# Kernel tuning notes

Hardware: AMD Instinct MI355X
Metric: run time of the kernel (lower is better)

## Reference

```python
import jax, jax.numpy as jnp
import numpy as np

NUM_HEADS = 8

def _ln(x, w, b, eps=1e-5):
    m = x.mean(-1, keepdims=True)
    v = ((x - m) ** 2).mean(-1, keepdims=True)
    return (x - m) / jnp.sqrt(v + eps) * w + b

def _l2n(x, axis=-1, eps=1e-12):
    n = jnp.linalg.norm(x, axis=axis, keepdims=True)
    return x / jnp.maximum(n, eps)

def setup_inputs() -> dict:
    key = jax.random.key(0)
    ks = jax.random.split(key, 30)
    B, N, C, nc, t = 2, 4096, 256, 150, 3
    Hh = Ww = 64
    hid = 4 * C
    s = 0.02
    inp = {}
    inp['x'] = jax.random.normal(ks[0], (B, N, C), jnp.float32)
    inp['z'] = jax.random.normal(ks[1], (B, nc, (t + 1) * N), jnp.float32)
    inp['mem'] = jax.random.normal(ks[2], (B * t, N, C), jnp.float32)
    inp['clustering_w'] = s * jax.random.normal(ks[3], (nc, C), jnp.float32)
    inp['prompt1'] = jax.random.normal(ks[4], (nc,), jnp.float32)
    inp['tdt1'] = jnp.eye(nc, dtype=jnp.float32) + s * jax.random.normal(ks[5], (nc, nc), jnp.float32)
    inp['prompt2'] = jax.random.normal(ks[6], (nc,), jnp.float32)
    inp['tdt2'] = jnp.eye(nc, dtype=jnp.float32) + s * jax.random.normal(ks[7], (nc, nc), jnp.float32)
    inp['sim_alpha'] = jnp.ones((1,), jnp.float32)
    inp['sim_beta'] = jnp.zeros((1,), jnp.float32)
    inp['q_w'] = s * jax.random.normal(ks[8], (C, C), jnp.float32)
    inp['q_b'] = s * jax.random.normal(ks[9], (C,), jnp.float32)
    inp['k_w'] = s * jax.random.normal(ks[10], (C, C), jnp.float32)
    inp['k_b'] = s * jax.random.normal(ks[11], (C,), jnp.float32)
    inp['v_w'] = s * jax.random.normal(ks[12], (C, C), jnp.float32)
    inp['v_b'] = s * jax.random.normal(ks[13], (C,), jnp.float32)
    inp['proj_w'] = s * jax.random.normal(ks[14], (C, C), jnp.float32)
    inp['proj_b'] = s * jax.random.normal(ks[15], (C,), jnp.float32)
    inp['norm_w'] = jnp.ones((C,), jnp.float32)
    inp['norm_b'] = jnp.zeros((C,), jnp.float32)
    inp['fc1_w'] = s * jax.random.normal(ks[16], (hid, C), jnp.float32)
    inp['fc1_b'] = s * jax.random.normal(ks[17], (hid,), jnp.float32)
    inp['dw_w'] = s * jax.random.normal(ks[18], (hid, 1, 3, 3), jnp.float32)
    inp['dw_b'] = s * jax.random.normal(ks[19], (hid,), jnp.float32)
    inp['fc2_w'] = s * jax.random.normal(ks[20], (C, hid), jnp.float32)
    inp['fc2_b'] = s * jax.random.normal(ks[21], (C,), jnp.float32)
    inp['H'] = Hh
    inp['W'] = Ww
    inp['t'] = t
    return inp

def _forward(x, z, mem, clustering_w, prompt1, tdt1, prompt2, tdt2, sim_alpha, sim_beta,
             q_w, q_b, k_w, k_b, v_w, v_b, proj_w, proj_b, norm_w, norm_b,
             fc1_w, fc1_b, dw_w, dw_b, fc2_w, fc2_b, H, W, t):
    B, N, C = x.shape
    nc = clustering_w.shape[0]
    res = x
    T = t + 1
    # cat memory frames with current frame: [(B*T), N, C]
    xf = jnp.concatenate([mem.reshape(B, t, N, C), x[:, None]], axis=1).reshape(B * T, N, C)
    # clustering head: (SRPS approximated as identity) 1x1 conv dim->num_clusters
    cl = jnp.einsum('bnc,kc->bkn', xf, clustering_w)            # [(B*T), nc, N]
    cl = cl.reshape(B, T, nc, N).transpose(0, 2, 1, 3).reshape(B, nc, T * N)
    # top-down prompt modulation of z and cluster logits
    zc = z.transpose(0, 2, 1)                                   # [B, T*N, nc]
    cos = _l2n(zc, -1) @ _l2n(prompt1[None, :, None], axis=1)   # [B, T*N, 1]
    zc = (zc * jnp.clip(cos, 0.0, 1.0)) @ tdt1
    clc = cl.transpose(0, 2, 1)
    cos = _l2n(clc, -1) @ _l2n(prompt2[None, :, None], axis=1)
    clc = (clc * jnp.clip(cos, 0.0, 1.0)) @ tdt2
    cluster_x_z = ((clc + zc) * 0.5).transpose(0, 2, 1)          # [B, nc, T*N]
    # inner_center: per-frame soft assignment -> cluster centers
    center = cluster_x_z.reshape(B, nc, T, N).transpose(0, 2, 1, 3)  # [B, T, nc, N]
    assigned_results = center
    soft = jax.nn.softmax(center, axis=-1)
    cx = xf.reshape(B, T, N, C)
    cen = jnp.einsum('btkn,btnc->btkc', soft, cx)               # [B, T, nc, C]
    last, prev = cen[:, -1], cen[:, :-1]                        # [B,nc,C], [B,t,nc,C]
    dot = jnp.einsum('bkc,btkc->btk', last, prev)
    denom = jnp.maximum(jnp.linalg.norm(last, axis=-1)[:, None] * jnp.linalg.norm(prev, axis=-1), 1e-8)
    gate = jax.nn.sigmoid(sim_beta + sim_alpha * (dot / denom))  # [B, t, nc]
    C_in = last + (gate[..., None] * prev).sum(axis=1)          # [B, nc, C]
    C_in = _ln(C_in, norm_w, norm_b)
    # cross attention: tokens query cluster centers
    hd = C // NUM_HEADS
    q = (res @ q_w.T + q_b) * (1.0 / np.sqrt(hd))
    k = C_in @ k_w.T + k_b
    v = C_in @ v_w.T + v_b
    q = q.reshape(B, N, NUM_HEADS, hd).transpose(0, 2, 1, 3)
    k = k.reshape(B, nc, NUM_HEADS, hd).transpose(0, 2, 1, 3)
    v = v.reshape(B, nc, NUM_HEADS, hd).transpose(0, 2, 1, 3)
    attn = jax.nn.softmax(jnp.einsum('bhnd,bhkd->bhnk', q, k), axis=-1)
    o = jnp.einsum('bhnk,bhkd->bhnd', attn, v).transpose(0, 2, 1, 3).reshape(B, N, C)
    o = o @ proj_w.T + proj_b
    out = res + _ln(o, norm_w, norm_b)
    # MLP with depthwise conv
    h = out @ fc1_w.T + fc1_b                                   # [B, N, 4C]
    hid = h.shape[-1]
    h_img = h.transpose(0, 2, 1).reshape(B, hid, H, W)
    h_img = jax.lax.conv_general_dilated(h_img, dw_w, (1, 1), 'SAME',
                                         feature_group_count=hid,
                                         dimension_numbers=('NCHW', 'OIHW', 'NCHW'))
    h_img = h_img + dw_b[None, :, None, None]
    h = h_img.reshape(B, hid, N).transpose(0, 2, 1)
    h = jax.nn.gelu(h, approximate=False) @ fc2_w.T + fc2_b
    out = out + _ln(h, norm_w, norm_b)
    return out, cluster_x_z, assigned_results

def reference(x, z, mem, clustering_w, prompt1, tdt1, prompt2, tdt2, sim_alpha, sim_beta,
              q_w, q_b, k_w, k_b, v_w, v_b, proj_w, proj_b, norm_w, norm_b,
              fc1_w, fc1_b, dw_w, dw_b, fc2_w, fc2_b, H, W, t):
    return _forward(x, z, mem, clustering_w, prompt1, tdt1, prompt2, tdt2, sim_alpha, sim_beta,
                    q_w, q_b, k_w, k_b, v_w, v_b, proj_w, proj_b, norm_w, norm_b,
                    fc1_w, fc1_b, dw_w, dw_b, fc2_w, fc2_b, H, W, t)
```

## Files before the change

kernel.cpp:

```cpp
#include <hip/hip_runtime.h>
#include <math.h>


typedef __attribute__((ext_vector_type(8))) short bf16x8;
typedef __attribute__((ext_vector_type(4))) short bf16x4;
typedef __attribute__((ext_vector_type(4))) float f32x4;

__device__ __forceinline__ short f2b(float f) {
  union { float f; unsigned int u; } c; c.f = f;
  unsigned int r = (c.u + 0x7fffu + ((c.u >> 16) & 1u)) >> 16;
  return (short)r;
}

__device__ __forceinline__ float bred_sum(float v, float* red) {
  int tid = threadIdx.x;
  red[tid] = v; __syncthreads();
  #pragma unroll
  for (int s = 128; s > 0; s >>= 1) {
    if (tid < s) red[tid] += red[tid + s];
    __syncthreads();
  }
  float r = red[0]; __syncthreads();
  return r;
}

__global__ __launch_bounds__(256) void gemm_mfma(
    const float* __restrict__ A, const float* __restrict__ W,
    const float* __restrict__ bias, float* __restrict__ out,
    int M, int N, int K, float alpha)
{
  __shared__ __align__(16) short As[64 * 72];
  __shared__ __align__(16) short Bs[64 * 72];
  const int tid = threadIdx.x;
  const int m0 = blockIdx.x * 64;
  const int n0 = blockIdx.y * 64;
  const int wave = tid >> 6;
  const int lane = tid & 63;
  const int wm = wave & 1, wn = wave >> 1;
  const int t16 = lane & 15;
  const int k8 = (lane >> 4) * 8;

  f32x4 acc[2][2];
  #pragma unroll
  for (int i = 0; i < 2; ++i)
    #pragma unroll
    for (int j = 0; j < 2; ++j)
      acc[i][j] = (f32x4){0.f, 0.f, 0.f, 0.f};

  const int sr = tid >> 2;
  const int sk = (tid & 3) * 16;

  for (int k0 = 0; k0 < K; k0 += 64) {
    {
      const float* ap = &A[(size_t)(m0 + sr) * K + k0 + sk];
      float4 v0 = *(const float4*)&ap[0];
      float4 v1 = *(const float4*)&ap[4];
      float4 v2 = *(const float4*)&ap[8];
      float4 v3 = *(const float4*)&ap[12];
      bf16x8 w0, w1;
      w0[0] = f2b(v0.x); w0[1] = f2b(v0.y); w0[2] = f2b(v0.z); w0[3] = f2b(v0.w);
      w0[4] = f2b(v1.x); w0[5] = f2b(v1.y); w0[6] = f2b(v1.z); w0[7] = f2b(v1.w);
      w1[0] = f2b(v2.x); w1[1] = f2b(v2.y); w1[2] = f2b(v2.z); w1[3] = f2b(v2.w);
      w1[4] = f2b(v3.x); w1[5] = f2b(v3.y); w1[6] = f2b(v3.z); w1[7] = f2b(v3.w);
      *(bf16x8*)&As[sr * 72 + sk] = w0;
      *(bf16x8*)&As[sr * 72 + sk + 8] = w1;
    }
    {
      const float* wp = &W[(size_t)(n0 + sr) * K + k0 + sk];
      float4 v0 = *(const float4*)&wp[0];
      float4 v1 = *(const float4*)&wp[4];
      float4 v2 = *(const float4*)&wp[8];
      float4 v3 = *(const float4*)&wp[12];
      bf16x8 w0, w1;
      w0[0] = f2b(v0.x); w0[1] = f2b(v0.y); w0[2] = f2b(v0.z); w0[3] = f2b(v0.w);
      w0[4] = f2b(v1.x); w0[5] = f2b(v1.y); w0[6] = f2b(v1.z); w0[7] = f2b(v1.w);
      w1[0] = f2b(v2.x); w1[1] = f2b(v2.y); w1[2] = f2b(v2.z); w1[3] = f2b(v2.w);
      w1[4] = f2b(v3.x); w1[5] = f2b(v3.y); w1[6] = f2b(v3.z); w1[7] = f2b(v3.w);
      *(bf16x8*)&Bs[sr * 72 + sk] = w0;
      *(bf16x8*)&Bs[sr * 72 + sk + 8] = w1;
    }
    __syncthreads();
    #pragma unroll
    for (int ks = 0; ks < 2; ++ks) {
      const int kofs = ks * 32 + k8;
      bf16x8 af0 = *(const bf16x8*)&As[(wm * 32 +  0 + t16) * 72 + kofs];
      bf16x8 af1 = *(const bf16x8*)&As[(wm * 32 + 16 + t16) * 72 + kofs];
      bf16x8 bf0 = *(const bf16x8*)&Bs[(wn * 32 +  0 + t16) * 72 + kofs];
      bf16x8 bf1 = *(const bf16x8*)&Bs[(wn * 32 + 16 + t16) * 72 + kofs];
      acc[0][0] = __builtin_amdgcn_mfma_f32_16x16x32_bf16(af0, bf0, acc[0][0], 0, 0, 0);
      acc[1][0] = __builtin_amdgcn_mfma_f32_16x16x32_bf16(af1, bf0, acc[1][0], 0, 0, 0);
      acc[0][1] = __builtin_amdgcn_mfma_f32_16x16x32_bf16(af0, bf1, acc[0][1], 0, 0, 0);
      acc[1][1] = __builtin_amdgcn_mfma_f32_16x16x32_bf16(af1, bf1, acc[1][1], 0, 0, 0);
    }
    __syncthreads();
  }
  const int r4 = (lane >> 4) * 4;
  #pragma unroll
  for (int ni = 0; ni < 2; ++ni) {
    const int gcol = n0 + wn * 32 + ni * 16 + t16;
    const float bb = bias[gcol];
    #pragma unroll
    for (int mi = 0; mi < 2; ++mi) {
      #pragma unroll
      for (int r = 0; r < 4; ++r) {
        const int gm = m0 + wm * 32 + mi * 16 + r4 + r;
        out[(size_t)gm * N + gcol] = alpha * (acc[mi][ni][r] + bb);
      }
    }
  }
}

__global__ __launch_bounds__(256) void gemm_ln_res(
    const float* __restrict__ A, const float* __restrict__ W,
    const float* __restrict__ bias, const float* __restrict__ res,
    const float* __restrict__ nw, const float* __restrict__ nb,
    float* __restrict__ dst, int K)
{
  __shared__ __align__(16) short As[16 * 72];
  __shared__ __align__(16) short Bs[256 * 72];
  __shared__ float red[16][4][2];
  const int tid = threadIdx.x;
  const int m0 = blockIdx.x * 16;
  const int wave = tid >> 6, lane = tid & 63;
  const int t16 = lane & 15, quad = lane >> 4, k8 = quad * 8;

  f32x4 acc[4];
  #pragma unroll
  for (int i = 0; i < 4; ++i) acc[i] = (f32x4){0.f, 0.f, 0.f, 0.f};

  const int sr = tid >> 2;
  const int sk = (tid & 3) * 16;
  const int arow = tid >> 4, akc = (tid & 15) * 4;

  for (int k0 = 0; k0 < K; k0 += 64) {
    {
      float4 v = *(const float4*)&A[(size_t)(m0 + arow) * K + k0 + akc];
      bf16x4 w;
      w[0] = f2b(v.x); w[1] = f2b(v.y); w[2] = f2b(v.z); w[3] = f2b(v.w);
      *(bf16x4*)&As[arow * 72 + akc] = w;
    }
    #pragma unroll
    for (int p = 0; p < 4; ++p) {
      const float* wp = &W[(size_t)(p * 64 + sr) * K + k0 + sk];
      float4 v0 = *(const float4*)&wp[0];
      float4 v1 = *(const float4*)&wp[4];
      float4 v2 = *(const float4*)&wp[8];
      float4 v3 = *(const float4*)&wp[12];
      bf16x8 w0, w1;
      w0[0] = f2b(v0.x); w0[1] = f2b(v0.y); w0[2] = f2b(v0.z); w0[3] = f2b(v0.w);
      w0[4] = f2b(v1.x); w0[5] = f2b(v1.y); w0[6] = f2b(v1.z); w0[7] = f2b(v1.w);
      w1[0] = f2b(v2.x); w1[1] = f2b(v2.y); w1[2] = f2b(v2.z); w1[3] = f2b(v2.w);
      w1[4] = f2b(v3.x); w1[5] = f2b(v3.y); w1[6] = f2b(v3.z); w1[7] = f2b(v3.w);
      *(bf16x8*)&Bs[(p * 64 + sr) * 72 + sk] = w0;
      *(bf16x8*)&Bs[(p * 64 + sr) * 72 + sk + 8] = w1;
    }
    __syncthreads();
    #pragma unroll
    for (int ks = 0; ks < 2; ++ks) {
      const int kofs = ks * 32 + k8;
      bf16x8 af = *(const bf16x8*)&As[t16 * 72 + kofs];
      #pragma unroll
      for (int ni = 0; ni < 4; ++ni) {
        bf16x8 bf = *(const bf16x8*)&Bs[(wave * 64 + ni * 16 + t16) * 72 + kofs];
        acc[ni] = __builtin_amdgcn_mfma_f32_16x16x32_bf16(af, bf, acc[ni], 0, 0, 0);
      }
    }
    __syncthreads();
  }

  const int gcolb = wave * 64;
  float val[4][4];
  float s[4] = {0.f, 0.f, 0.f, 0.f}, s2[4] = {0.f, 0.f, 0.f, 0.f};
  #pragma unroll
  for (int ni = 0; ni < 4; ++ni) {
    const float bb = bias[gcolb + ni * 16 + t16];
    #pragma unroll
    for (int r = 0; r < 4; ++r) {
      float v = acc[ni][r] + bb;
      val[ni][r] = v;
      s[r] += v;
      s2[r] = fmaf(v, v, s2[r]);
    }
  }
  #pragma unroll
  for (int off = 1; off < 16; off <<= 1) {
    #pragma unroll
    for (int r = 0; r < 4; ++r) {
      s[r] += __shfl_xor(s[r], off);
      s2[r] += __shfl_xor(s2[r], off);
    }
  }
  if (t16 == 0) {
    #pragma unroll
    for (int r = 0; r < 4; ++r) {
      red[quad * 4 + r][wave][0] = s[r];
      red[quad * 4 + r][wave][1] = s2[r];
    }
  }
  __syncthreads();
  float mu[4], inv[4];
  #pragma unroll
  for (int r = 0; r < 4; ++r) {
    const int row = quad * 4 + r;
    float st  = red[row][0][0] + red[row][1][0] + red[row][2][0] + red[row][3][0];
    float st2 = red[row][0][1] + red[row][1][1] + red[row][2][1] + red[row][3][1];
    float m = st * (1.f / 256.f);
    mu[r] = m;
    inv[r] = rsqrtf(st2 * (1.f / 256.f) - m * m + 1e-5f);
  }
  #pragma unroll
  for (int ni = 0; ni < 4; ++ni) {
    const int gcol = gcolb + ni * 16 + t16;
    const float wc = nw[gcol], bc = nb[gcol];
    #pragma unroll
    for (int r = 0; r < 4; ++r) {
      const int gm = m0 + quad * 4 + r;
      dst[(size_t)gm * 256 + gcol] =
          res[(size_t)gm * 256 + gcol] + (val[ni][r] - mu[r]) * inv[r] * wc + bc;
    }
  }
}

__global__ __launch_bounds__(256) void prep_bt(
    const float* __restrict__ cw, const float* __restrict__ tdt2, const float* __restrict__ tdt1,
    short* __restrict__ cwb, short* __restrict__ TT)
{
  int idx = blockIdx.x * 256 + threadIdx.x;
  if (idx < 160 * 256) {
    int kc = idx >> 8, k = idx & 255;
    float v = (kc < 150) ? cw[kc * 256 + k] : 0.f;
    cwb[idx] = f2b(v);
  }
  if (idx < 160 * 320) {
    int kc = idx / 320, kk = idx - kc * 320;
    float t = 0.f;
    if (kc < 150) {
      if (kk < 150) t = tdt2[kk * 150 + kc];
      else if (kk >= 160 && kk < 310) t = tdt1[(kk - 160) * 150 + kc];
    }
    TT[idx] = f2b(t);
  }
}

__global__ __launch_bounds__(256) void xf_t(
    const float* __restrict__ x, const float* __restrict__ mem, short* __restrict__ xfT)
{
  __shared__ float tile[64][257];
  const int bt = blockIdx.y;
  const int n0 = blockIdx.x * 64;
  const int b = bt >> 2, ti = bt & 3;
  const float* xf = (ti < 3) ? (mem + (size_t)(b * 3 + ti) * 4096 * 256)
                             : (x + (size_t)b * 4096 * 256);
  const int tid = threadIdx.x;
  const int r = tid >> 2, cofs = (tid & 3) * 64;
  const float* src = xf + (size_t)(n0 + r) * 256 + cofs;
  #pragma unroll
  for (int i = 0; i < 16; ++i) {
    float4 v = *(const float4*)&src[i * 4];
    tile[r][cofs + i * 4 + 0] = v.x;
    tile[r][cofs + i * 4 + 1] = v.y;
    tile[r][cofs + i * 4 + 2] = v.z;
    tile[r][cofs + i * 4 + 3] = v.w;
  }
  __syncthreads();
  short* dst = xfT + ((size_t)bt * 256 + tid) * 4096 + n0;
  #pragma unroll
  for (int seg = 0; seg < 8; ++seg) {
    bf16x8 w;
    #pragma unroll
    for (int j = 0; j < 8; ++j) w[j] = f2b(tile[seg * 8 + j][tid]);
    *(bf16x8*)&dst[seg * 8] = w;
  }
}

__global__ __launch_bounds__(256) void fused_csz(
    const float* __restrict__ x, const float* __restrict__ mem, const float* __restrict__ z,
    const short* __restrict__ cwb, const short* __restrict__ TT,
    const float* __restrict__ p1, const float* __restrict__ p2,
    float* __restrict__ csz, float* __restrict__ asg)
{
  __shared__ __align__(16) short Acatile[64 * 328];
  __shared__ float p1s[160], p2s[160];
  __shared__ float sred[4][16][9];
  __shared__ float czs[64];
  const int tid = threadIdx.x;
  const int r0 = blockIdx.x * 64;
  const int b = r0 >> 14;
  const int mmg = r0 & 16383;
  const int ti = mmg >> 12, nn = mmg & 4095;
  const float* Ab = ((ti < 3) ? (mem + (size_t)(b * 3 + ti) * 4096 * 256)
                              : (x + (size_t)b * 4096 * 256)) + (size_t)nn * 256;
  const int wave = tid >> 6, lane = tid & 63;
  const int t16 = lane & 15, quad = lane >> 4, k8 = quad * 8;

  const int kr = tid >> 4, c4 = (tid & 15) * 4;
  float4 zv[10];
  #pragma unroll
  for (int it = 0; it < 10; ++it) {
    const int k = it * 16 + kr;
    zv[it] = make_float4(0.f, 0.f, 0.f, 0.f);
    if (k < 150) zv[it] = *(const float4*)&z[((size_t)b * 150 + k) * 16384 + mmg + c4];
  }
  if (tid < 160) {
    p2s[tid] = (tid < 150) ? p2[tid] : 0.f;
    p1s[tid] = (tid < 150) ? p1[tid] : 0.f;
  }

  f32x4 acc[10];
  #pragma unroll
  for (int i = 0; i < 10; ++i) acc[i] = (f32x4){0.f, 0.f, 0.f, 0.f};
  {
    const float* ap = Ab + (size_t)(wave * 16 + t16) * 256 + k8;
    const short* bp = cwb + t16 * 256 + k8;
    #pragma unroll 2
    for (int ks = 0; ks < 8; ++ks) {
      float4 v0 = *(const float4*)&ap[ks * 32];
      float4 v1 = *(const float4*)&ap[ks * 32 + 4];
      bf16x8 a;
      a[0] = f2b(v0.x); a[1] = f2b(v0.y); a[2] = f2b(v0.z); a[3] = f2b(v0.w);
      a[4] = f2b(v1.x); a[5] = f2b(v1.y); a[6] = f2b(v1.z); a[7] = f2b(v1.w);
      #pragma unroll
      for (int nf = 0; nf < 10; ++nf) {
        bf16x8 bv = *(const bf16x8*)&bp[nf * 4096 + ks * 32];
        acc[nf] = __builtin_amdgcn_mfma_f32_16x16x32_bf16(a, bv, acc[nf], 0, 0, 0);
      }
    }
  }
  __syncthreads();

  {
    float d[4] = {0.f, 0.f, 0.f, 0.f}, s[4] = {0.f, 0.f, 0.f, 0.f};
    float pn = 0.f;
    #pragma unroll
    for (int nf = 0; nf < 10; ++nf) {
      float a2 = p2s[nf * 16 + t16];
      pn += a2 * a2;
      #pragma unroll
      for (int r = 0; r < 4; ++r) {
        float v = acc[nf][r];
        d[r] = fmaf(v, a2, d[r]);
        s[r] = fmaf(v, v, s[r]);
      }
    }
    #pragma unroll
    for (int off = 1; off < 16; off <<= 1) {
      pn += __shfl_xor(pn, off);
      #pragma unroll
      for (int r = 0; r < 4; ++r) {
        d[r] += __shfl_xor(d[r], off);
        s[r] += __shfl_xor(s[r], off);
      }
    }
    const float spn = fmaxf(sqrtf(pn), 1e-12f);
    float cs[4];
    #pragma unroll
    for (int r = 0; r < 4; ++r) {
      float c = d[r] / (fmaxf(sqrtf(s[r]), 1e-12f) * spn);
      cs[r] = fminf(fmaxf(c, 0.f), 1.f);
    }
    #pragma unroll
    for (int nf = 0; nf < 10; ++nf)
      #pragma unroll
      for (int r = 0; r < 4; ++r)
        Acatile[(wave * 16 + quad * 4 + r) * 328 + nf * 16 + t16] = f2b(acc[nf][r] * cs[r]);
  }

  {
    float d[4] = {0.f, 0.f, 0.f, 0.f}, sv[4] = {0.f, 0.f, 0.f, 0.f};
    float pn = 0.f;
    #pragma unroll
    for (int it = 0; it < 10; ++it) {
      const int k = it * 16 + kr;
      const float a = p1s[k];
      d[0] = fmaf(zv[it].x, a, d[0]); d[1] = fmaf(zv[it].y, a, d[1]);
      d[2] = fmaf(zv[it].z, a, d[2]); d[3] = fmaf(zv[it].w, a, d[3]);
      sv[0] = fmaf(zv[it].x, zv[it].x, sv[0]); sv[1] = fmaf(zv[it].y, zv[it].y, sv[1]);
      sv[2] = fmaf(zv[it].z, zv[it].z, sv[2]); sv[3] = fmaf(zv[it].w, zv[it].w, sv[3]);
      pn = fmaf(a, a, pn);
    }
    #pragma unroll
    for (int off = 16; off < 64; off <<= 1) {
      pn += __shfl_xor(pn, off);
      #pragma unroll
      for (int r = 0; r < 4; ++r) {
        d[r] += __shfl_xor(d[r], off);
        sv[r] += __shfl_xor(sv[r], off);
      }
    }
    if ((lane >> 4) == 0) {
      #pragma unroll
      for (int r = 0; r < 4; ++r) {
        sred[wave][lane][r] = d[r];
        sred[wave][lane][4 + r] = sv[r];
      }
      sred[wave][lane][8] = pn;
    }
  }
  __syncthreads();
  if (tid < 64) {
    const int cg = tid >> 2, r = tid & 3;
    float dd = 0.f, ss = 0.f, pp = 0.f;
    #pragma unroll
    for (int w = 0; w < 4; ++w) {
      dd += sred[w][cg][r];
      ss += sred[w][cg][4 + r];
      pp += sred[w][cg][8];
    }
    float c = dd / (fmaxf(sqrtf(ss), 1e-12f) * fmaxf(sqrtf(pp), 1e-12f));
    czs[tid] = fminf(fmaxf(c, 0.f), 1.f);
  }
  __syncthreads();
  {
    const float cz0 = czs[c4 + 0], cz1 = czs[c4 + 1], cz2 = czs[c4 + 2], cz3 = czs[c4 + 3];
    #pragma unroll
    for (int it = 0; it < 10; ++it) {
      const int k = it * 16 + kr;
      Acatile[(c4 + 0) * 328 + 160 + k] = f2b(zv[it].x * cz0);
      Acatile[(c4 + 1) * 328 + 160 + k] = f2b(zv[it].y * cz1);
      Acatile[(c4 + 2) * 328 + 160 + k] = f2b(zv[it].z * cz2);
      Acatile[(c4 + 3) * 328 + 160 + k] = f2b(zv[it].w * cz3);
    }
  }
  __syncthreads();

  {
    const int wm = wave & 1, wn = wave >> 1;
    f32x4 c2[2][5];
    #pragma unroll
    for (int i = 0; i < 2; ++i)
      #pragma unroll
      for (int j = 0; j < 5; ++j)
        c2[i][j] = (f32x4){0.f, 0.f, 0.f, 0.f};
    const short* bp = TT + (size_t)(wn * 80 + t16) * 320 + k8;
    #pragma unroll 2
    for (int ks = 0; ks < 10; ++ks) {
      bf16x8 a0 = *(const bf16x8*)&Acatile[(wm * 32 + t16) * 328 + ks * 32 + k8];
      bf16x8 a1 = *(const bf16x8*)&Acatile[(wm * 32 + 16 + t16) * 328 + ks * 32 + k8];
      #pragma unroll
      for (int nf = 0; nf < 5; ++nf) {
        bf16x8 bv = *(const bf16x8*)&bp[nf * 5120 + ks * 32];
        c2[0][nf] = __builtin_amdgcn_mfma_f32_16x16x32_bf16(a0, bv, c2[0][nf], 0, 0, 0);
        c2[1][nf] = __builtin_amdgcn_mfma_f32_16x16x32_bf16(a1, bv, c2[1][nf], 0, 0, 0);
      }
    }
    #pragma unroll
    for (int nf = 0; nf < 5; ++nf) {
      const int kc = wn * 80 + nf * 16 + t16;
      if (kc < 150) {
        #pragma unroll
        for (int mf = 0; mf < 2; ++mf) {
          const int moff = wm * 32 + mf * 16 + quad * 4;
          float4 r4;
          r4.x = 0.5f * c2[mf][nf][0];
          r4.y = 0.5f * c2[mf][nf][1];
          r4.z = 0.5f * c2[mf][nf][2];
          r4.w = 0.5f * c2[mf][nf][3];
          *(float4*)&csz[((size_t)b * 150 + kc) * 16384 + mmg + moff] = r4;
          *(float4*)&asg[(((size_t)b * 4 + ti) * 150 + kc) * 4096 + nn + moff] = r4;
        }
      }
    }
  }
}

__global__ __launch_bounds__(256) void softmax_stats_e(
    const float* __restrict__ csz, float* __restrict__ lr_, short* __restrict__ ecsz)
{
  __shared__ float wred[8];
  const int row = blockIdx.x;
  const int bt = row / 150, k = row - bt * 150;
  const int b = bt >> 2, ti = bt & 3;
  const float* p = csz + ((size_t)b * 150 + k) * 16384 + ti * 4096;
  const int base = threadIdx.x * 16;
  float4 v[4];
  #pragma unroll
  for (int i = 0; i < 4; ++i) v[i] = *(const float4*)&p[base + i * 4];
  float mx = -1e30f;
  #pragma unroll
  for (int i = 0; i < 4; ++i)
    mx = fmaxf(mx, fmaxf(fmaxf(v[i].x, v[i].y), fmaxf(v[i].z, v[i].w)));
  #pragma unroll
  for (int off = 1; off < 64; off <<= 1) mx = fmaxf(mx, __shfl_xor(mx, off));
  const int wave = threadIdx.x >> 6, lane = threadIdx.x & 63;
  if (lane == 0) wred[wave] = mx;
  __syncthreads();
  mx = fmaxf(fmaxf(wred[0], wred[1]), fmaxf(wred[2], wred[3]));
  const float L = 1.4426950408889634f;
  float s = 0.f;
  bf16x8 e0, e1;
  #pragma unroll
  for (int i = 0; i < 2; ++i) {
    float a = exp2f((v[i].x - mx) * L);
    float bq = exp2f((v[i].y - mx) * L);
    float cq = exp2f((v[i].z - mx) * L);
    float dq = exp2f((v[i].w - mx) * L);
    s += a + bq + cq + dq;
    e0[i * 4 + 0] = f2b(a); e0[i * 4 + 1] = f2b(bq); e0[i * 4 + 2] = f2b(cq); e0[i * 4 + 3] = f2b(dq);
  }
  #pragma unroll
  for (int i = 2; i < 4; ++i) {
    float a = exp2f((v[i].x - mx) * L);
    float bq = exp2f((v[i].y - mx) * L);
    float cq = exp2f((v[i].z - mx) * L);
    float dq = exp2f((v[i].w - mx) * L);
    s += a + bq + cq + dq;
    e1[(i - 2) * 4 + 0] = f2b(a); e1[(i - 2) * 4 + 1] = f2b(bq);
    e1[(i - 2) * 4 + 2] = f2b(cq); e1[(i - 2) * 4 + 3] = f2b(dq);
  }
  #pragma unroll
  for (int off = 1; off < 64; off <<= 1) s += __shfl_xor(s, off);
  if (lane == 0) wred[4 + wave] = s;
  __syncthreads();
  short* er = ecsz + ((size_t)bt * 160 + k) * 4096 + base;
  *(bf16x8*)&er[0] = e0;
  *(bf16x8*)&er[8] = e1;
  if (threadIdx.x == 0) lr_[row] = wred[4] + wred[5] + wred[6] + wred[7];
}

__global__ __launch_bounds__(256) void gemm_cen_at(
    const short* __restrict__ ecsz, const short* __restrict__ xfT,
    float* __restrict__ cen)
{
  __shared__ __align__(16) short As[160 * 136];
  const int tid = threadIdx.x;
  const int chalf = blockIdx.x;
  const int bt = blockIdx.y;
  const int sp = blockIdx.z;
  const int n0 = sp * 128;
  const int wave = tid >> 6, lane = tid & 63;
  const int t16 = lane & 15, quad = lane >> 4, k8 = quad * 8;
  const int cbase = chalf * 128 + wave * 32;

  f32x4 acc[10][2];
  #pragma unroll
  for (int i = 0; i < 10; ++i) {
    acc[i][0] = (f32x4){0.f, 0.f, 0.f, 0.f};
    acc[i][1] = (f32x4){0.f, 0.f, 0.f, 0.f};
  }

  const short* erow = ecsz + (size_t)bt * 160 * 4096 + n0;
  #pragma unroll
  for (int p = 0; p < 10; ++p) {
    const int g = p * 256 + tid;
    const int row = g >> 4;
    const int col8 = (g & 15) * 8;
    *(bf16x8*)&As[row * 136 + col8] = *(const bf16x8*)&erow[(size_t)row * 4096 + col8];
  }
  __syncthreads();
  const short* xrow = xfT + (size_t)bt * 256 * 4096 + n0;
  #pragma unroll
  for (int kc = 0; kc < 4; ++kc) {
    bf16x8 b0 = *(const bf16x8*)&xrow[(size_t)(cbase + t16) * 4096 + kc * 32 + k8];
    bf16x8 b1 = *(const bf16x8*)&xrow[(size_t)(cbase + 16 + t16) * 4096 + kc * 32 + k8];
    #pragma unroll
    for (int mt = 0; mt < 10; ++mt) {
      bf16x8 aA = *(const bf16x8*)&As[(mt * 16 + t16) * 136 + kc * 32 + k8];
      acc[mt][0] = __builtin_amdgcn_mfma_f32_16x16x32_bf16(aA, b0, acc[mt][0], 0, 0, 0);
      acc[mt][1] = __builtin_amdgcn_mfma_f32_16x16x32_bf16(aA, b1, acc[mt][1], 0, 0, 0);
    }
  }
  #pragma unroll
  for (int mt = 0; mt < 10; ++mt) {
    #pragma unroll
    for (int r = 0; r < 4; ++r) {
      const int grow = mt * 16 + quad * 4 + r;
      if (grow < 150) {
        atomicAdd(&cen[((size_t)bt * 150 + grow) * 256 + cbase + t16], acc[mt][0][r]);
        atomicAdd(&cen[((size_t)bt * 150 + grow) * 256 + cbase + 16 + t16], acc[mt][1][r]);
      }
    }
  }
}

__global__ __launch_bounds__(256) void gate_ln(
    const float* __restrict__ cen, const float* __restrict__ lr_,
    const float* __restrict__ alpha_, const float* __restrict__ beta_,
    const float* __restrict__ nw, const float* __restrict__ nb, float* __restrict__ cin)
{
  __shared__ float red[256];
  int bk = blockIdx.x;
  int b = bk / 150, k = bk % 150;
  int c = threadIdx.x;
  const float* base = cen + ((size_t)b * 4 * 150) * 256;
  const float* lrb = lr_ + (size_t)b * 4 * 150;
  float lc  = base[((size_t)3 * 150 + k) * 256 + c] / lrb[3 * 150 + k];
  float p0  = base[((size_t)0 * 150 + k) * 256 + c] / lrb[0 * 150 + k];
  float p1v = base[((size_t)1 * 150 + k) * 256 + c] / lrb[1 * 150 + k];
  float p2v = base[((size_t)2 * 150 + k) * 256 + c] / lrb[2 * 150 + k];
  float nl = bred_sum(lc * lc, red);
  float q0 = bred_sum(p0 * p0, red);
  float q1 = bred_sum(p1v * p1v, red);
  float q2 = bred_sum(p2v * p2v, red);
  float d0 = bred_sum(lc * p0, red);
  float d1 = bred_sum(lc * p1v, red);
  float d2 = bred_sum(lc * p2v, red);
  float al = alpha_[0], be = beta_[0];
  float snl = sqrtf(nl);
  float g0 = 1.f / (1.f + expf(-(be + al * (d0 / fmaxf(snl * sqrtf(q0), 1e-8f)))));
  float g1 = 1.f / (1.f + expf(-(be + al * (d1 / fmaxf(snl * sqrtf(q1), 1e-8f)))));
  float g2 = 1.f / (1.f + expf(-(be + al * (d2 / fmaxf(snl * sqrtf(q2), 1e-8f)))));
  float ci = lc + g0 * p0 + g1 * p1v + g2 * p2v;
  float mu = bred_sum(ci, red) * (1.f / 256.f);
  float df = ci - mu;
  float var = bred_sum(df * df, red) * (1.f / 256.f);
  cin[(size_t)bk * 256 + c] = df * rsqrtf(var + 1e-5f) * nw[c] + nb[c];
}

__global__ __launch_bounds__(256) void gemm_nt(
    const float* __restrict__ A, const float* __restrict__ W,
    const float* __restrict__ bias, float* __restrict__ out,
    int M, int N, int K, float alpha)
{
  __shared__ __align__(16) float As[16][132];
  __shared__ __align__(16) float Ws[16][68];
  const int tid = threadIdx.x;
  const int m0 = blockIdx.x * 128;
  const int n0 = blockIdx.y * 64;
  const int tm = tid & 15;
  const int tn = tid >> 4;
  float acc[8][4];
  #pragma unroll
  for (int i = 0; i < 8; ++i)
    #pragma unroll
    for (int j = 0; j < 4; ++j) acc[i][j] = 0.f;

  const int lr = tid >> 2;
  const int lk = (tid & 3) * 4;

  for (int k0 = 0; k0 < K; k0 += 16) {
    #pragma unroll
    for (int p = 0; p < 2; ++p) {
      int r = lr + p * 64;
      int gm = m0 + r;
      float4 v = make_float4(0.f, 0.f, 0.f, 0.f);
      if (gm < M) v = *(const float4*)&A[(size_t)gm * K + k0 + lk];
      As[lk + 0][r] = v.x; As[lk + 1][r] = v.y; As[lk + 2][r] = v.z; As[lk + 3][r] = v.w;
    }
    {
      float4 v = *(const float4*)&W[(size_t)(n0 + lr) * K + k0 + lk];
      Ws[lk + 0][lr] = v.x; Ws[lk + 1][lr] = v.y; Ws[lk + 2][lr] = v.z; Ws[lk + 3][lr] = v.w;
    }
    __syncthreads();
    #pragma unroll
    for (int kk = 0; kk < 16; ++kk) {
      float4 a0 = *(const float4*)&As[kk][tm * 8];
      float4 a1 = *(const float4*)&As[kk][tm * 8 + 4];
      float4 w0 = *(const float4*)&Ws[kk][tn * 4];
      float av[8] = {a0.x, a0.y, a0.z, a0.w, a1.x, a1.y, a1.z, a1.w};
      float wv[4] = {w0.x, w0.y, w0.z, w0.w};
      #pragma unroll
      for (int i = 0; i < 8; ++i)
        #pragma unroll
        for (int j = 0; j < 4; ++j)
          acc[i][j] = fmaf(av[i], wv[j], acc[i][j]);
    }
    __syncthreads();
  }
  float4 bv = *(const float4*)&bias[n0 + tn * 4];
  float bb[4] = {bv.x, bv.y, bv.z, bv.w};
  #pragma unroll
  for (int i = 0; i < 8; ++i) {
    int gm = m0 + tm * 8 + i;
    if (gm >= M) continue;
    float4 r;
    r.x = alpha * (acc[i][0] + bb[0]);
    r.y = alpha * (acc[i][1] + bb[1]);
    r.z = alpha * (acc[i][2] + bb[2]);
    r.w = alpha * (acc[i][3] + bb[3]);
    *(float4*)&out[(size_t)gm * N + n0 + tn * 4] = r;
  }
}

__global__ __launch_bounds__(256) void attn_mfma(
    const float* __restrict__ q, const float* __restrict__ ks, const float* __restrict__ vs,
    float* __restrict__ o)
{
  __shared__ __align__(16) short Ps[128 * 168];
  __shared__ __align__(16) short VT[32 * 168];
  __shared__ float lrow[128];
  const int tid = threadIdx.x;
  const int bid = blockIdx.x;
  const int ntile = bid & 31;
  const int bh = bid >> 5;
  const int b = bh >> 3, h = bh & 7;
  const int n0 = ntile * 128;
  const int wave = tid >> 6, lane = tid & 63;
  const int t16 = lane & 15, quad = lane >> 4;
  const int k8 = quad * 8;
  const int wr = wave * 32;

  for (int i = tid; i < 5120; i += 256) {
    int d = i / 160, kc = i - d * 160;
    VT[d * 168 + kc] = (kc < 150) ? f2b(vs[((size_t)b * 150 + kc) * 256 + h * 32 + d]) : (short)0;
  }

  bf16x8 aQ[2];
  #pragma unroll
  for (int mt = 0; mt < 2; ++mt) {
    const float* qp = &q[((size_t)b * 4096 + n0 + wr + mt * 16 + t16) * 256 + h * 32 + k8];
    float4 v0 = *(const float4*)&qp[0];
    float4 v1 = *(const float4*)&qp[4];
    bf16x8 w;
    w[0] = f2b(v0.x); w[1] = f2b(v0.y); w[2] = f2b(v0.z); w[3] = f2b(v0.w);
    w[4] = f2b(v1.x); w[5] = f2b(v1.y); w[6] = f2b(v1.z); w[7] = f2b(v1.w);
    aQ[mt] = w;
  }

  f32x4 s[2][10];
  #pragma unroll
  for (int ct = 0; ct < 10; ++ct) {
    const int c = ct * 16 + t16;
    bf16x8 bK = {0, 0, 0, 0, 0, 0, 0, 0};
    if (c < 150) {
      const float* kp = &ks[((size_t)b * 150 + c) * 256 + h * 32 + k8];
      float4 v0 = *(const float4*)&kp[0];
      float4 v1 = *(const float4*)&kp[4];
      bK[0] = f2b(v0.x); bK[1] = f2b(v0.y); bK[2] = f2b(v0.z); bK[3] = f2b(v0.w);
      bK[4] = f2b(v1.x); bK[5] = f2b(v1.y); bK[6] = f2b(v1.z); bK[7] = f2b(v1.w);
    }
    f32x4 zero = (f32x4){0.f, 0.f, 0.f, 0.f};
    s[0][ct] = __builtin_amdgcn_mfma_f32_16x16x32_bf16(aQ[0], bK, zero, 0, 0, 0);
    s[1][ct] = __builtin_amdgcn_mfma_f32_16x16x32_bf16(aQ[1], bK, zero, 0, 0, 0);
  }

  #pragma unroll
  for (int mt = 0; mt < 2; ++mt) {
    #pragma unroll
    for (int r = 0; r < 4; ++r) {
      float mx = -1e30f;
      #pragma unroll
      for (int ct = 0; ct < 10; ++ct) {
        float v = s[mt][ct][r];
        if (ct == 9 && t16 >= 6) { v = -1e30f; s[mt][ct][r] = v; }
        mx = fmaxf(mx, v);
      }
      mx = fmaxf(mx, __shfl_xor(mx, 1));
      mx = fmaxf(mx, __shfl_xor(mx, 2));
      mx = fmaxf(mx, __shfl_xor(mx, 4));
      mx = fmaxf(mx, __shfl_xor(mx, 8));
      float ls = 0.f;
      #pragma unroll
      for (int ct = 0; ct < 10; ++ct) {
        float e = expf(s[mt][ct][r] - mx);
        s[mt][ct][r] = e;
        ls += e;
      }
      ls += __shfl_xor(ls, 1);
      ls += __shfl_xor(ls, 2);
      ls += __shfl_xor(ls, 4);
      ls += __shfl_xor(ls, 8);
      if (t16 == 0) lrow[wr + mt * 16 + quad * 4 + r] = 1.f / ls;
      #pragma unroll
      for (int ct = 0; ct < 10; ++ct)
        Ps[(wr + mt * 16 + quad * 4 + r) * 168 + ct * 16 + t16] = f2b(s[mt][ct][r]);
    }
  }
  __syncthreads();

  f32x4 oacc[2][2];
  #pragma unroll
  for (int i = 0; i < 2; ++i)
    #pragma unroll
    for (int j = 0; j < 2; ++j)
      oacc[i][j] = (f32x4){0.f, 0.f, 0.f, 0.f};
  #pragma unroll
  for (int kstep = 0; kstep < 5; ++kstep) {
    bf16x8 bV0 = *(const bf16x8*)&VT[( 0 + t16) * 168 + kstep * 32 + k8];
    bf16x8 bV1 = *(const bf16x8*)&VT[(16 + t16) * 168 + kstep * 32 + k8];
    #pragma unroll
    for (int mt = 0; mt < 2; ++mt) {
      bf16x8 aP = *(const bf16x8*)&Ps[(wr + mt * 16 + t16) * 168 + kstep * 32 + k8];
      oacc[mt][0] = __builtin_amdgcn_mfma_f32_16x16x32_bf16(aP, bV0, oacc[mt][0], 0, 0, 0);
      oacc[mt][1] = __builtin_amdgcn_mfma_f32_16x16x32_bf16(aP, bV1, oacc[mt][1], 0, 0, 0);
    }
  }
  #pragma unroll
  for (int mt = 0; mt < 2; ++mt) {
    #pragma unroll
    for (int nt = 0; nt < 2; ++nt) {
      const int d = nt * 16 + t16;
      #pragma unroll
      for (int r = 0; r < 4; ++r) {
        const int row = wr + mt * 16 + quad * 4 + r;
        o[((size_t)b * 4096 + n0 + row) * 256 + h * 32 + d] = oacc[mt][nt][r] * lrow[row];
      }
    }
  }
}

__global__ __launch_bounds__(256) void conv_wt(
    const float* __restrict__ w, float* __restrict__ wt)
{
  int i = blockIdx.x * 256 + threadIdx.x;
  if (i < 9216) {
    int ch = i / 9, tap = i - ch * 9;
    wt[tap * 1024 + ch] = w[i];
  }
}

__global__ __launch_bounds__(256) void conv_gelu(
    const float* __restrict__ h, const float* __restrict__ wt, const float* __restrict__ bias,
    float* __restrict__ hc)
{
  const int bid = blockIdx.x;
  const int xg = bid & 15;
  const int y  = (bid >> 4) & 63;
  const int b  = bid >> 10;
  const int x0 = xg * 4;
  const int c4 = threadIdx.x * 4;
  const float* hb = h + ((size_t)b * 4096) * 1024 + c4;

  float4 tap[3][6];
  #pragma unroll
  for (int dy = 0; dy < 3; ++dy) {
    const int yy = y + dy - 1;
    #pragma unroll
    for (int dx = 0; dx < 6; ++dx) {
      const int xv = x0 + dx - 1;
      tap[dy][dx] = make_float4(0.f, 0.f, 0.f, 0.f);
      if (yy >= 0 && yy <= 63 && xv >= 0 && xv <= 63)
        tap[dy][dx] = *(const float4*)&hb[(size_t)(yy * 64 + xv) * 1024];
    }
  }
  float4 wv[3][3];
  #pragma unroll
  for (int dy = 0; dy < 3; ++dy)
    #pragma unroll
    for (int dx = 0; dx < 3; ++dx)
      wv[dy][dx] = *(const float4*)&wt[(dy * 3 + dx) * 1024 + c4];
  const float4 bv = *(const float4*)&bias[c4];

  #pragma unroll
  for (int p = 0; p < 4; ++p) {
    float4 acc = bv;
    #pragma unroll
    for (int dy = 0; dy < 3; ++dy) {
      #pragma unroll
      for (int dx = 0; dx < 3; ++dx) {
        const float4 hv = tap[dy][p + dx];
        const float4 w = wv[dy][dx];
        acc.x = fmaf(hv.x, w.x, acc.x);
        acc.y = fmaf(hv.y, w.y, acc.y);
        acc.z = fmaf(hv.z, w.z, acc.z);
        acc.w = fmaf(hv.w, w.w, acc.w);
      }
    }
    float4 g;
    g.x = 0.5f * acc.x * (1.f + erff(acc.x * 0.70710678118654752f));
    g.y = 0.5f * acc.y * (1.f + erff(acc.y * 0.70710678118654752f));
    g.z = 0.5f * acc.z * (1.f + erff(acc.z * 0.70710678118654752f));
    g.w = 0.5f * acc.w * (1.f + erff(acc.w * 0.70710678118654752f));
    *(float4*)&hc[((size_t)b * 4096 + y * 64 + x0 + p) * 1024 + c4] = g;
  }
}

extern "C" void kernel_launch(void* const* d_in, const int* in_sizes, int n_in,
                              void* d_out, int out_size, void* d_ws, size_t ws_size,
                              hipStream_t stream)
{
  (void)in_sizes; (void)n_in; (void)out_size; (void)ws_size;
  const float* x    = (const float*)d_in[0];
  const float* z    = (const float*)d_in[1];
  const float* mem  = (const float*)d_in[2];
  const float* cw   = (const float*)d_in[3];
  const float* p1   = (const float*)d_in[4];
  const float* tdt1 = (const float*)d_in[5];
  const float* p2   = (const float*)d_in[6];
  const float* tdt2 = (const float*)d_in[7];
  const float* sal  = (const float*)d_in[8];
  const float* sbe  = (const float*)d_in[9];
  const float* q_w  = (const float*)d_in[10];
  const float* q_b  = (const float*)d_in[11];
  const float* k_w  = (const float*)d_in[12];
  const float* k_b  = (const float*)d_in[13];
  const float* v_w  = (const float*)d_in[14];
  const float* v_b  = (const float*)d_in[15];
  const float* pj_w = (const float*)d_in[16];
  const float* pj_b = (const float*)d_in[17];
  const float* nw   = (const float*)d_in[18];
  const float* nb   = (const float*)d_in[19];
  const float* f1w  = (const float*)d_in[20];
  const float* f1b  = (const float*)d_in[21];
  const float* dww  = (const float*)d_in[22];
  const float* dwb  = (const float*)d_in[23];
  const float* f2w  = (const float*)d_in[24];
  const float* f2b_ = (const float*)d_in[25];

  float* out = (float*)d_out;
  float* csz = out + 2097152;
  float* asg = csz + 4915200;

  float* ws    = (float*)d_ws;
  short* ecsz  = (short*)ws;
  short* TT    = (short*)(ws + 5242880);
  short* cwb   = (short*)(ws + 5275648);
  float* lr_   = ws + 5308416;
  float* cen   = ws + 5310816;
  float* cin   = ws + 5618016;
  float* q     = ws + 5694816;
  float* ksb   = ws + 7791968;
  float* vsb   = ws + 7868768;
  float* o     = ws + 7945568;
  short* xfT   = (short*)(ws + 10042720);
  float* h     = ws;
  float* hc    = ws + 8388608;
  float* out1  = ws + 18874368;
  float* wt    = ws + 20971520;

  dim3 blk(256);
  prep_bt<<<dim3(200), blk, 0, stream>>>(cw, tdt2, tdt1, cwb, TT);
  xf_t<<<dim3(64, 8), blk, 0, stream>>>(x, mem, xfT);
  fused_csz<<<dim3(512), blk, 0, stream>>>(x, mem, z, cwb, TT, p1, p2, csz, asg);
  softmax_stats_e<<<dim3(1200), blk, 0, stream>>>(csz, lr_, ecsz);
  hipMemsetAsync(cen, 0, (size_t)1200 * 256 * sizeof(float), stream);
  gemm_cen_at<<<dim3(2, 8, 32), blk, 0, stream>>>(ecsz, xfT, cen);
  gate_ln<<<dim3(300), blk, 0, stream>>>(cen, lr_, sal, sbe, nw, nb, cin);
  gemm_mfma<<<dim3(128, 4), blk, 0, stream>>>(x, q_w, q_b, q, 8192, 256, 256, 0.17677669529663687f);
  gemm_nt<<<dim3(3, 4), blk, 0, stream>>>(cin, k_w, k_b, ksb, 300, 256, 256, 1.f);
  gemm_nt<<<dim3(3, 4), blk, 0, stream>>>(cin, v_w, v_b, vsb, 300, 256, 256, 1.f);
  attn_mfma<<<dim3(512), blk, 0, stream>>>(q, ksb, vsb, o);
  gemm_ln_res<<<dim3(512), blk, 0, stream>>>(o, pj_w, pj_b, x, nw, nb, out1, 256);
  gemm_mfma<<<dim3(128, 16), blk, 0, stream>>>(out1, f1w, f1b, h, 8192, 1024, 256, 1.f);
  conv_wt<<<dim3(36), blk, 0, stream>>>(dww, wt);
  conv_gelu<<<dim3(2048), blk, 0, stream>>>(h, wt, dwb, hc);
  gemm_ln_res<<<dim3(512), blk, 0, stream>>>(hc, f2w, f2b_, out1, nw, nb, out, 1024);
}
```

Before: 453.5 us.

## Pre-convert projection and fc2 weights to bf16; load MFMA operands directly from global

The prep kernel now also converts the proj and fc2 weight matrices to bf16 once per call. gemm_ln_res drops its shared-memory staging and barriers, and each wave reads its A and B fragments straight from global memory (A as fp32, converted in registers). This removes the per-block fp32-to-bf16 weight conversion and the LDS round trips. In exchange every block rereads the weights from global/L2 without reuse through LDS, and prep_bt launches more blocks.

```diff
diff --git a/kernel.cpp b/kernel.cpp
--- a/kernel.cpp
+++ b/kernel.cpp
@@ -3,7 +3,6 @@
 
 
 typedef __attribute__((ext_vector_type(8))) short bf16x8;
-typedef __attribute__((ext_vector_type(4))) short bf16x4;
 typedef __attribute__((ext_vector_type(4))) float f32x4;
 
 __device__ __forceinline__ short f2b(float f) {
@@ -111,13 +110,11 @@
 }
 
 __global__ __launch_bounds__(256) void gemm_ln_res(
-    const float* __restrict__ A, const float* __restrict__ W,
+    const float* __restrict__ A, const short* __restrict__ Wb,
     const float* __restrict__ bias, const float* __restrict__ res,
     const float* __restrict__ nw, const float* __restrict__ nb,
     float* __restrict__ dst, int K)
 {
-  __shared__ __align__(16) short As[16 * 72];
-  __shared__ __align__(16) short Bs[256 * 72];
   __shared__ float red[16][4][2];
   const int tid = threadIdx.x;
   const int m0 = blockIdx.x * 16;
@@ -128,44 +125,21 @@
   #pragma unroll
   for (int i = 0; i < 4; ++i) acc[i] = (f32x4){0.f, 0.f, 0.f, 0.f};
 
-  const int sr = tid >> 2;
-  const int sk = (tid & 3) * 16;
-  const int arow = tid >> 4, akc = (tid & 15) * 4;
-
-  for (int k0 = 0; k0 < K; k0 += 64) {
-    {
-      float4 v = *(const float4*)&A[(size_t)(m0 + arow) * K + k0 + akc];
-      bf16x4 w;
-      w[0] = f2b(v.x); w[1] = f2b(v.y); w[2] = f2b(v.z); w[3] = f2b(v.w);
-      *(bf16x4*)&As[arow * 72 + akc] = w;
-    }
-    #pragma unroll
-    for (int p = 0; p < 4; ++p) {
-      const float* wp = &W[(size_t)(p * 64 + sr) * K + k0 + sk];
-      float4 v0 = *(const float4*)&wp[0];
-      float4 v1 = *(const float4*)&wp[4];
-      float4 v2 = *(const float4*)&wp[8];
-      float4 v3 = *(const float4*)&wp[12];
-      bf16x8 w0, w1;
-      w0[0] = f2b(v0.x); w0[1] = f2b(v0.y); w0[2] = f2b(v0.z); w0[3] = f2b(v0.w);
-      w0[4] = f2b(v1.x); w0[5] = f2b(v1.y); w0[6] = f2b(v1.z); w0[7] = f2b(v1.w);
-      w1[0] = f2b(v2.x); w1[1] = f2b(v2.y); w1[2] = f2b(v2.z); w1[3] = f2b(v2.w);
-      w1[4] = f2b(v3.x); w1[5] = f2b(v3.y); w1[6] = f2b(v3.z); w1[7] = f2b(v3.w);
-      *(bf16x8*)&Bs[(p * 64 + sr) * 72 + sk] = w0;
-      *(bf16x8*)&Bs[(p * 64 + sr) * 72 + sk + 8] = w1;
-    }
-    __syncthreads();
-    #pragma unroll
-    for (int ks = 0; ks < 2; ++ks) {
-      const int kofs = ks * 32 + k8;
-      bf16x8 af = *(const bf16x8*)&As[t16 * 72 + kofs];
-      #pragma unroll
-      for (int ni = 0; ni < 4; ++ni) {
-        bf16x8 bf = *(const bf16x8*)&Bs[(wave * 64 + ni * 16 + t16) * 72 + kofs];
-        acc[ni] = __builtin_amdgcn_mfma_f32_16x16x32_bf16(af, bf, acc[ni], 0, 0, 0);
-      }
-    }
-    __syncthreads();
+  const float* ap = &A[(size_t)(m0 + t16) * K + k8];
+  const short* wp = &Wb[(size_t)(wave * 64 + t16) * K + k8];
+
+  #pragma unroll 4
+  for (int k0 = 0; k0 < K; k0 += 32) {
+    float4 v0 = *(const float4*)&ap[k0];
+    float4 v1 = *(const float4*)&ap[k0 + 4];
+    bf16x8 af;
+    af[0] = f2b(v0.x); af[1] = f2b(v0.y); af[2] = f2b(v0.z); af[3] = f2b(v0.w);
+    af[4] = f2b(v1.x); af[5] = f2b(v1.y); af[6] = f2b(v1.z); af[7] = f2b(v1.w);
+    #pragma unroll
+    for (int ni = 0; ni < 4; ++ni) {
+      bf16x8 bv = *(const bf16x8*)&wp[(size_t)ni * 16 * K + k0];
+      acc[ni] = __builtin_amdgcn_mfma_f32_16x16x32_bf16(af, bv, acc[ni], 0, 0, 0);
+    }
   }
 
   const int gcolb = wave * 64;
@@ -223,7 +197,9 @@
 
 __global__ __launch_bounds__(256) void prep_bt(
     const float* __restrict__ cw, const float* __restrict__ tdt2, const float* __restrict__ tdt1,
-    short* __restrict__ cwb, short* __restrict__ TT)
+    const float* __restrict__ pjw, const float* __restrict__ f2w,
+    short* __restrict__ cwb, short* __restrict__ TT,
+    short* __restrict__ pjwb, short* __restrict__ f2wb)
 {
   int idx = blockIdx.x * 256 + threadIdx.x;
   if (idx < 160 * 256) {
@@ -240,6 +216,8 @@
     }
     TT[idx] = f2b(t);
   }
+  if (idx < 65536) pjwb[idx] = f2b(pjw[idx]);
+  if (idx < 262144) f2wb[idx] = f2b(f2w[idx]);
 }
 
 __global__ __launch_bounds__(256) void xf_t(
@@ -906,9 +884,11 @@
   float* hc    = ws + 8388608;
   float* out1  = ws + 18874368;
   float* wt    = ws + 20971520;
+  short* pjwb  = (short*)(ws + 20980736);
+  short* f2wb  = (short*)(ws + 21013504);
 
   dim3 blk(256);
-  prep_bt<<<dim3(200), blk, 0, stream>>>(cw, tdt2, tdt1, cwb, TT);
+  prep_bt<<<dim3(1024), blk, 0, stream>>>(cw, tdt2, tdt1, pj_w, f2w, cwb, TT, pjwb, f2wb);
   xf_t<<<dim3(64, 8), blk, 0, stream>>>(x, mem, xfT);
   fused_csz<<<dim3(512), blk, 0, stream>>>(x, mem, z, cwb, TT, p1, p2, csz, asg);
   softmax_stats_e<<<dim3(1200), blk, 0, stream>>>(csz, lr_, ecsz);
@@ -919,9 +899,9 @@
   gemm_nt<<<dim3(3, 4), blk, 0, stream>>>(cin, k_w, k_b, ksb, 300, 256, 256, 1.f);
   gemm_nt<<<dim3(3, 4), blk, 0, stream>>>(cin, v_w, v_b, vsb, 300, 256, 256, 1.f);
   attn_mfma<<<dim3(512), blk, 0, stream>>>(q, ksb, vsb, o);
-  gemm_ln_res<<<dim3(512), blk, 0, stream>>>(o, pj_w, pj_b, x, nw, nb, out1, 256);
+  gemm_ln_res<<<dim3(512), blk, 0, stream>>>(o, pjwb, pj_b, x, nw, nb, out1, 256);
   gemm_mfma<<<dim3(128, 16), blk, 0, stream>>>(out1, f1w, f1b, h, 8192, 1024, 256, 1.f);
   conv_wt<<<dim3(36), blk, 0, stream>>>(dww, wt);
   conv_gelu<<<dim3(2048), blk, 0, stream>>>(h, wt, dwb, hc);
-  gemm_ln_res<<<dim3(512), blk, 0, stream>>>(hc, f2w, f2b_, out1, nw, nb, out, 1024);
-}
+  gemm_ln_res<<<dim3(512), blk, 0, stream>>>(hc, f2wb, f2b_, out1, nw, nb, out, 1024);
+}
```

Result: no change. 447.7 us (-1.3%).
